# Performance work log

Measured on AMD Instinct MI355X. Metric: run time of the kernel, lower is better.

## Reference

```python
import jax, jax.numpy as jnp
import numpy as np

V = 50000      # word vocab
CV = 63        # char vocab (60 chars + 3 tags)
HW = 512       # word hidden size
HC = 256       # char hidden size
NLW = 2        # word lstm layers
NLC = 2        # char lstm layers
L = 12         # chars in the word


def _lstm_layers(x, H, C, Wih, Whh, bih, bhh):
    """One time-step of a multi-layer LSTM (PyTorch gate order i,f,g,o).
    x: [1, D], H/C: [nl, 1, D]. Returns (top_h, newH, newC)."""
    nl = Wih.shape[0]
    newH, newC = [], []
    inp = x
    for l in range(nl):
        gates = inp @ Wih[l].T + H[l] @ Whh[l].T + bih[l] + bhh[l]  # [1, 4D]
        i, f, g, o = jnp.split(gates, 4, axis=-1)
        i = jax.nn.sigmoid(i)
        f = jax.nn.sigmoid(f)
        g = jnp.tanh(g)
        o = jax.nn.sigmoid(o)
        c = f * C[l] + i * g
        h = o * jnp.tanh(c)
        newH.append(h)
        newC.append(c)
        inp = h
    return inp, jnp.stack(newH), jnp.stack(newC)


def setup_inputs() -> dict:
    key = jax.random.key(0)
    ks = jax.random.split(key, 20)
    sW = 1.0 / np.sqrt(HW)
    sC = 1.0 / np.sqrt(HC)
    return {
        "x_word": jax.random.randint(ks[0], (1,), 0, V),
        "x_char": jax.random.randint(ks[1], (L,), 0, CV),
        "h_word_h": jax.random.normal(ks[2], (NLW, 1, HW), jnp.float32),
        "h_word_c": jax.random.normal(ks[3], (NLW, 1, HW), jnp.float32),
        "h_char_h": jax.random.normal(ks[4], (NLC, 1, HC), jnp.float32),
        "h_char_c": jax.random.normal(ks[5], (NLC, 1, HC), jnp.float32),
        "word_emb": jax.random.normal(ks[6], (V, HW), jnp.float32),
        "word_Wih": jax.random.normal(ks[7], (NLW, 4 * HW, HW), jnp.float32) * sW,
        "word_Whh": jax.random.normal(ks[8], (NLW, 4 * HW, HW), jnp.float32) * sW,
        "word_bih": jax.random.normal(ks[9], (NLW, 4 * HW), jnp.float32) * sW,
        "word_bhh": jax.random.normal(ks[10], (NLW, 4 * HW), jnp.float32) * sW,
        "dec_W": jax.random.normal(ks[11], (V, HW), jnp.float32) * sW,
        "dec_b": jax.random.normal(ks[12], (V,), jnp.float32) * sW,
        "char_emb": jax.random.normal(ks[13], (CV, HC), jnp.float32),
        "char_Wih": jax.random.normal(ks[14], (NLC, 4 * HC, HC), jnp.float32) * sC,
        "char_Whh": jax.random.normal(ks[15], (NLC, 4 * HC, HC), jnp.float32) * sC,
        "char_bih": jax.random.normal(ks[16], (NLC, 4 * HC), jnp.float32) * sC,
        "char_bhh": jax.random.normal(ks[17], (NLC, 4 * HC), jnp.float32) * sC,
        "char_to_embedding": jax.random.normal(ks[18], (HW, HC), jnp.float32),
        "g_w": jax.random.normal(ks[19], (HW,), jnp.float32) * sW,
        "g_b": jax.random.normal(jax.random.fold_in(key, 99), (1,), jnp.float32),
    }


def reference(x_word, x_char, h_word_h, h_word_c, h_char_h, h_char_c,
              word_emb, word_Wih, word_Whh, word_bih, word_bhh,
              dec_W, dec_b,
              char_emb, char_Wih, char_Whh, char_bih, char_bhh,
              char_to_embedding, g_w, g_b):
    # character-level recurrence over the word's characters
    def char_step(carry, cidx):
        H, C = carry
        xc = char_emb[cidx][None, :]  # [1, HC]
        _, H, C = _lstm_layers(xc, H, C, char_Wih, char_Whh, char_bih, char_bhh)
        return (H, C), None

    (h_char_h, h_char_c), _ = jax.lax.scan(char_step, (h_char_h, h_char_c), x_char)

    # note: original uses h_char[1] (the CELL state) of the last layer
    x_c = char_to_embedding @ h_char_c[-1].T          # [HW, 1]
    x_w = word_emb[x_word[0]][None, :]                # [1, HW]
    g = jax.nn.relu(jnp.dot(g_w, x_w[0]) + g_b[0])    # scalar gate
    x = (1.0 - g) * x_w + g * x_c.T                   # [1, HW]

    y, h_word_h, h_word_c = _lstm_layers(x, h_word_h, h_word_c,
                                         word_Wih, word_Whh, word_bih, word_bhh)
    y = y @ dec_W.T + dec_b                           # [1, V]
    return y, h_word_h, h_word_c, h_char_h, h_char_c
```

## Files before the change

kernel.cpp:

```cpp
#include <hip/hip_runtime.h>
#include <stdint.h>


static __device__ __forceinline__ float dot4(float4 w, const float* p){
    return w.x*p[0] + w.y*p[1] + w.z*p[2] + w.w*p[3];
}
static __device__ __forceinline__ float sigf(float x){ return 1.0f / (1.0f + __expf(-x)); }
static __device__ __forceinline__ float tanhf_(float x){
    x = fminf(fmaxf(x, -15.0f), 15.0f);
    float e = __expf(2.0f * x);
    return (e - 1.0f) / (e + 1.0f);
}


__global__ __launch_bounds__(256) void k_char(
    int t,
    const int* __restrict__ x_char,
    const float* __restrict__ hch, const float* __restrict__ hcc,
    const float* __restrict__ char_emb,
    const float* __restrict__ cWih, const float* __restrict__ cWhh,
    const float* __restrict__ cbih, const float* __restrict__ cbhh,
    const float* __restrict__ word_emb, const int* __restrict__ x_word,
    const float* __restrict__ g_w, const float* __restrict__ g_b,
    float* __restrict__ ws)
{
    const int tid = threadIdx.x;
    const int bx = blockIdx.x;

    if (bx == 64){
        if (t == 0){
            __shared__ float sw[4];
            const size_t wbase = (size_t)x_word[0] * 512;
            float p = g_w[2*tid]   * word_emb[wbase + 2*tid]
                    + g_w[2*tid+1] * word_emb[wbase + 2*tid+1];
            #pragma unroll
            for (int m = 32; m >= 1; m >>= 1) p += __shfl_xor(p, m, 64);
            if ((tid & 63) == 0) sw[tid >> 6] = p;
            __syncthreads();
            if (tid == 0){
                float gg = sw[0] + sw[1] + sw[2] + sw[3] + g_b[0];
                ws[3072] = fmaxf(gg, 0.0f);
            }
        }
        return;
    }

    __shared__ float sH1[256];
    __shared__ float sH2[256];
    __shared__ float sE[256];
    __shared__ float sg1[16], sg2[16];

    float* h1b = ws;
    float* h2b = ws + 512;
    float* c1  = ws + 1024;
    float* c2  = ws + 1280;

    sH1[tid] = (t == 0) ? hch[tid] : h1b[(t & 1)*256 + tid];
    if (t >= 1) sH2[tid] = (t == 1) ? hch[256 + tid] : h2b[((t-1) & 1)*256 + tid];
    if (t < 12) sE[tid] = char_emb[x_char[t]*256 + tid];
    __syncthreads();

    const int rg = tid >> 4;
    const int lane16 = tid & 15;
    const int gate = rg & 3;
    const int uu = rg >> 2;
    const int u = (bx << 2) + uu;
    const int row = (gate << 8) + u;

    float a1 = 0.f, a2 = 0.f;
    if (t < 12){
        const float4* wi = (const float4*)(cWih + (size_t)row*256) + lane16*4;
        const float4* wh = (const float4*)(cWhh + (size_t)row*256) + lane16*4;
        const float* xp = sE  + lane16*16;
        const float* hp = sH1 + lane16*16;
        #pragma unroll
        for (int j = 0; j < 4; ++j) a1 += dot4(wi[j], xp + 4*j) + dot4(wh[j], hp + 4*j);
    }
    if (t >= 1){
        const size_t r2 = (size_t)(1024 + row);
        const float4* wi = (const float4*)(cWih + r2*256) + lane16*4;
        const float4* wh = (const float4*)(cWhh + r2*256) + lane16*4;
        const float* xp = sH1 + lane16*16;
        const float* hp = sH2 + lane16*16;
        #pragma unroll
        for (int j = 0; j < 4; ++j) a2 += dot4(wi[j], xp + 4*j) + dot4(wh[j], hp + 4*j);
    }
    #pragma unroll
    for (int m = 8; m >= 1; m >>= 1){
        a1 += __shfl_xor(a1, m, 64);
        a2 += __shfl_xor(a2, m, 64);
    }
    if (lane16 == 0){
        if (t < 12) sg1[rg] = a1 + cbih[row]        + cbhh[row];
        if (t >= 1) sg2[rg] = a2 + cbih[1024 + row] + cbhh[1024 + row];
    }
    __syncthreads();

    if (tid < 4){
        if (t < 12){
            int uh = (bx << 2) + tid;
            float gi = sigf(sg1[tid*4+0]);
            float gf = sigf(sg1[tid*4+1]);
            float gg = tanhf_(sg1[tid*4+2]);
            float go = sigf(sg1[tid*4+3]);
            float cp = (t == 0) ? hcc[uh] : c1[uh];
            float c = gf * cp + gi * gg;
            c1[uh] = c;
            h1b[((t+1) & 1)*256 + uh] = go * tanhf_(c);
        }
    } else if (tid < 8){
        if (t >= 1){
            int q = tid - 4;
            int uh = (bx << 2) + q;
            float gi = sigf(sg2[q*4+0]);
            float gf = sigf(sg2[q*4+1]);
            float gg = tanhf_(sg2[q*4+2]);
            float go = sigf(sg2[q*4+3]);
            float cp = (t == 1) ? hcc[256 + uh] : c2[uh];
            float c = gf * cp + gi * gg;
            c2[uh] = c;
            h2b[(t & 1)*256 + uh] = go * tanhf_(c);
        }
    }
}

__global__ __launch_bounds__(256) void k_mix(
    const float* __restrict__ cte, float* __restrict__ ws,
    float* __restrict__ out)
{
    const int tid = threadIdx.x;
    const int bx = blockIdx.x;
    __shared__ float sC2[256];
    sC2[tid] = ws[1280 + tid];
    __syncthreads();

    if (tid < 4){
        int uh = (bx << 2) + tid;
        out[52048 + uh]       = ws[uh];
        out[52048 + 256 + uh] = ws[512 + uh];
        out[52560 + uh]       = ws[1024 + uh];
        out[52560 + 256 + uh] = ws[1280 + uh];
    }
    const int rr = tid >> 5;
    const int lane32 = tid & 31;
    const int row = (bx << 3) + rr;
    const float4* wp = (const float4*)(cte + (size_t)row*256) + lane32*2;
    float acc = dot4(wp[0], sC2 + lane32*8) + dot4(wp[1], sC2 + lane32*8 + 4);
    #pragma unroll
    for (int m = 16; m >= 1; m >>= 1) acc += __shfl_xor(acc, m, 64);
    if (lane32 == 0) ws[1536 + row] = acc;
}

__global__ __launch_bounds__(256) void k_word(
    int l,
    const float* __restrict__ hwh, const float* __restrict__ hwc,
    const float* __restrict__ word_emb, const int* __restrict__ x_word,
    const float* __restrict__ wWih, const float* __restrict__ wWhh,
    const float* __restrict__ wbih, const float* __restrict__ wbhh,
    float* __restrict__ ws, float* __restrict__ out)
{
    const int tid = threadIdx.x;
    const int bx = blockIdx.x;
    __shared__ float sX[512];
    __shared__ float sg[32];

    if (l == 0){
        const size_t wbase = (size_t)x_word[0] * 512;
        float g = ws[3072];
        sX[2*tid]   = (1.0f - g) * word_emb[wbase + 2*tid]   + g * ws[1536 + 2*tid];
        sX[2*tid+1] = (1.0f - g) * word_emb[wbase + 2*tid+1] + g * ws[1536 + 2*tid+1];
    } else {
        sX[2*tid]   = ws[2048 + 2*tid];
        sX[2*tid+1] = ws[2048 + 2*tid+1];
    }
    __syncthreads();

    const int rg8 = tid >> 3;
    const int lane8 = tid & 7;
    const int gate = rg8 & 3;
    const int uu = rg8 >> 2;
    const int uw = (bx << 3) + uu;
    const int row = (gate << 9) + uw;
    const size_t rf = (size_t)(l*2048 + row);

    const float4* wi = (const float4*)(wWih + rf*512) + lane8*16;
    const float4* wh = (const float4*)(wWhh + rf*512) + lane8*16;
    const float4* hv = (const float4*)(hwh + l*512) + lane8*16;
    const float* xp = sX + lane8*64;
    float acc = 0.f;
    #pragma unroll
    for (int j = 0; j < 16; ++j){
        float4 h4 = hv[j];
        acc += dot4(wi[j], xp + 4*j);
        float4 w4 = wh[j];
        acc += w4.x*h4.x + w4.y*h4.y + w4.z*h4.z + w4.w*h4.w;
    }
    #pragma unroll
    for (int m = 4; m >= 1; m >>= 1) acc += __shfl_xor(acc, m, 64);
    if (lane8 == 0) sg[rg8] = acc + wbih[rf] + wbhh[rf];
    __syncthreads();

    if (tid < 8){
        int u2 = (bx << 3) + tid;
        float gi = sigf(sg[tid*4+0]);
        float gf = sigf(sg[tid*4+1]);
        float gg = tanhf_(sg[tid*4+2]);
        float go = sigf(sg[tid*4+3]);
        float c = gf * hwc[l*512 + u2] + gi * gg;
        float h = go * tanhf_(c);
        ws[2048 + l*512 + u2] = h;
        out[50000 + l*512 + u2] = h;
        out[51024 + l*512 + u2] = c;
    }
}

__global__ __launch_bounds__(256) void k_dec(
    const float* __restrict__ dec_W, const float* __restrict__ dec_b,
    const float* __restrict__ h2, float* __restrict__ out)
{
    const int lane = threadIdx.x & 63;
    const int wid = (blockIdx.x * blockDim.x + threadIdx.x) >> 6;
    const int nw = (gridDim.x * blockDim.x) >> 6;
    const float4* hp = (const float4*)h2 + lane*2;
    float4 ha = hp[0], hb = hp[1];
    float hx0[4] = {ha.x, ha.y, ha.z, ha.w};
    float hx1[4] = {hb.x, hb.y, hb.z, hb.w};
    for (int r = wid; r < 50000; r += nw){
        const float4* wp = (const float4*)(dec_W + (size_t)r*512) + lane*2;
        float acc = dot4(wp[0], hx0) + dot4(wp[1], hx1);
        #pragma unroll
        for (int m = 32; m >= 1; m >>= 1) acc += __shfl_xor(acc, m, 64);
        if (lane == 0) out[r] = acc + dec_b[r];
    }
}

extern "C" void kernel_launch(void* const* d_in, const int* in_sizes, int n_in,
                              void* d_out, int out_size, void* d_ws, size_t ws_size,
                              hipStream_t stream)
{
    const int*   x_word   = (const int*)d_in[0];
    const int*   x_char   = (const int*)d_in[1];
    const float* hwh      = (const float*)d_in[2];
    const float* hwc      = (const float*)d_in[3];
    const float* hch      = (const float*)d_in[4];
    const float* hcc      = (const float*)d_in[5];
    const float* word_emb = (const float*)d_in[6];
    const float* wWih     = (const float*)d_in[7];
    const float* wWhh     = (const float*)d_in[8];
    const float* wbih     = (const float*)d_in[9];
    const float* wbhh     = (const float*)d_in[10];
    const float* dec_W    = (const float*)d_in[11];
    const float* dec_b    = (const float*)d_in[12];
    const float* char_emb = (const float*)d_in[13];
    const float* cWih     = (const float*)d_in[14];
    const float* cWhh     = (const float*)d_in[15];
    const float* cbih     = (const float*)d_in[16];
    const float* cbhh     = (const float*)d_in[17];
    const float* cte      = (const float*)d_in[18];
    const float* g_w      = (const float*)d_in[19];
    const float* g_b      = (const float*)d_in[20];

    float* ws = (float*)d_ws;
    float* out = (float*)d_out;

    for (int t = 0; t <= 12; ++t){
        hipLaunchKernelGGL(k_char, dim3(65), dim3(256), 0, stream,
            t, x_char, hch, hcc, char_emb, cWih, cWhh, cbih, cbhh,
            word_emb, x_word, g_w, g_b, ws);
    }
    hipLaunchKernelGGL(k_mix, dim3(64), dim3(256), 0, stream, cte, ws, out);
    hipLaunchKernelGGL(k_word, dim3(64), dim3(256), 0, stream,
        0, hwh, hwc, word_emb, x_word, wWih, wWhh, wbih, wbhh, ws, out);
    hipLaunchKernelGGL(k_word, dim3(64), dim3(256), 0, stream,
        1, hwh, hwc, word_emb, x_word, wWih, wWhh, wbih, wbhh, ws, out);
    hipLaunchKernelGGL(k_dec, dim3(625), dim3(256), 0, stream,
        dec_W, dec_b, ws + 2560, out);
}
```

Measured before the change: 329.7 us.

## Fuse all stages into one persistent kernel with grid barriers and decoder prefetch

Replaces the 17 separate launches (13 char steps, mix, two word layers, decoder) with one persistent kernel of 256 blocks. The first 64 blocks run the recurrent chain and synchronise through atomic grid barriers in workspace. The other 192 blocks stream the whole decoder weight matrix to warm the cache, then spin on a flag before everyone does the decoder GEMV. This removes launch overhead and overlaps the decoder weight fetch with the serial LSTM work. It relies on all blocks being co-resident and adds spin-wait costs; the prefetch only helps if the matrix (about 100MB) stays in the last-level cache.

```diff
diff --git a/kernel.cpp b/kernel.cpp
--- a/kernel.cpp
+++ b/kernel.cpp
@@ -1,6 +1,11 @@
 #include <hip/hip_runtime.h>
 #include <stdint.h>
 
+
+#define NCHAR 64
+#define NBLK  256
+#define BAR_I 3072
+#define FLAG_SLOT 20
 
 static __device__ __forceinline__ float dot4(float4 w, const float* p){
     return w.x*p[0] + w.y*p[1] + w.z*p[2] + w.w*p[3];
@@ -12,220 +17,253 @@
     return (e - 1.0f) / (e + 1.0f);
 }
 
-
-__global__ __launch_bounds__(256) void k_char(
-    int t,
-    const int* __restrict__ x_char,
-    const float* __restrict__ hch, const float* __restrict__ hcc,
-    const float* __restrict__ char_emb,
-    const float* __restrict__ cWih, const float* __restrict__ cWhh,
-    const float* __restrict__ cbih, const float* __restrict__ cbhh,
-    const float* __restrict__ word_emb, const int* __restrict__ x_word,
-    const float* __restrict__ g_w, const float* __restrict__ g_b,
-    float* __restrict__ ws)
+static __device__ __forceinline__ void gbar(int* bar, int slot, int n){
+    __syncthreads();
+    if (threadIdx.x == 0){
+        __hip_atomic_fetch_add(bar + slot, 1, __ATOMIC_RELEASE, __HIP_MEMORY_SCOPE_AGENT);
+        while (__hip_atomic_load(bar + slot, __ATOMIC_RELAXED, __HIP_MEMORY_SCOPE_AGENT) < n)
+            __builtin_amdgcn_s_sleep(1);
+        (void)__hip_atomic_load(bar + slot, __ATOMIC_ACQUIRE, __HIP_MEMORY_SCOPE_AGENT);
+    }
+    __syncthreads();
+}
+
+
+__global__ __launch_bounds__(256) void k_fused(
+    const int* x_word, const int* x_char,
+    const float* hwh, const float* hwc, const float* hch, const float* hcc,
+    const float* word_emb, const float* wWih, const float* wWhh,
+    const float* wbih, const float* wbhh,
+    const float* dec_W, const float* dec_b,
+    const float* char_emb, const float* cWih, const float* cWhh,
+    const float* cbih, const float* cbhh,
+    const float* cte, const float* g_w, const float* g_b,
+    float* ws, int* bar, float* out)
 {
     const int tid = threadIdx.x;
     const int bx = blockIdx.x;
 
-    if (bx == 64){
-        if (t == 0){
-            __shared__ float sw[4];
-            const size_t wbase = (size_t)x_word[0] * 512;
+    __shared__ float sH1[256], sH2[256], sE[256];
+    __shared__ float sg1[16], sg2[16];
+    __shared__ float sX[512];
+    __shared__ float sgw[32];
+    __shared__ float sw4[4];
+    __shared__ float s_g;
+
+    if (bx < NCHAR){
+        float* h1b = ws;
+        float* h2b = ws + 512;
+        float* c1  = ws + 1024;
+        float* c2  = ws + 1280;
+
+        const int rg = tid >> 4;
+        const int lane16 = tid & 15;
+        const int gate = rg & 3;
+        const int uu = rg >> 2;
+        const int u = (bx << 2) + uu;
+        const int row = (gate << 8) + u;
+
+        for (int t = 0; t <= 12; ++t){
+            sH1[tid] = (t == 0) ? hch[tid] : h1b[(t & 1)*256 + tid];
+            if (t >= 1) sH2[tid] = (t == 1) ? hch[256 + tid] : h2b[((t-1) & 1)*256 + tid];
+            if (t < 12) sE[tid] = char_emb[x_char[t]*256 + tid];
+            __syncthreads();
+
+            float a1 = 0.f, a2 = 0.f;
+            if (t < 12){
+                const float4* wi = (const float4*)(cWih + (size_t)row*256) + lane16*4;
+                const float4* wh = (const float4*)(cWhh + (size_t)row*256) + lane16*4;
+                const float* xp = sE  + lane16*16;
+                const float* hp = sH1 + lane16*16;
+                #pragma unroll
+                for (int j = 0; j < 4; ++j) a1 += dot4(wi[j], xp + 4*j) + dot4(wh[j], hp + 4*j);
+            }
+            if (t >= 1){
+                const size_t r2 = (size_t)(1024 + row);
+                const float4* wi = (const float4*)(cWih + r2*256) + lane16*4;
+                const float4* wh = (const float4*)(cWhh + r2*256) + lane16*4;
+                const float* xp = sH1 + lane16*16;
+                const float* hp = sH2 + lane16*16;
+                #pragma unroll
+                for (int j = 0; j < 4; ++j) a2 += dot4(wi[j], xp + 4*j) + dot4(wh[j], hp + 4*j);
+            }
+            #pragma unroll
+            for (int m = 8; m >= 1; m >>= 1){
+                a1 += __shfl_xor(a1, m, 64);
+                a2 += __shfl_xor(a2, m, 64);
+            }
+            if (lane16 == 0){
+                if (t < 12) sg1[rg] = a1 + cbih[row]        + cbhh[row];
+                if (t >= 1) sg2[rg] = a2 + cbih[1024 + row] + cbhh[1024 + row];
+            }
+            __syncthreads();
+
+            if (tid < 4){
+                if (t < 12){
+                    int uh = (bx << 2) + tid;
+                    float gi = sigf(sg1[tid*4+0]);
+                    float gf = sigf(sg1[tid*4+1]);
+                    float gg = tanhf_(sg1[tid*4+2]);
+                    float go = sigf(sg1[tid*4+3]);
+                    float cp = (t == 0) ? hcc[uh] : c1[uh];
+                    float c = gf * cp + gi * gg;
+                    c1[uh] = c;
+                    h1b[((t+1) & 1)*256 + uh] = go * tanhf_(c);
+                }
+            } else if (tid < 8){
+                if (t >= 1){
+                    int q = tid - 4;
+                    int uh = (bx << 2) + q;
+                    float gi = sigf(sg2[q*4+0]);
+                    float gf = sigf(sg2[q*4+1]);
+                    float gg = tanhf_(sg2[q*4+2]);
+                    float go = sigf(sg2[q*4+3]);
+                    float cp = (t == 1) ? hcc[256 + uh] : c2[uh];
+                    float c = gf * cp + gi * gg;
+                    c2[uh] = c;
+                    h2b[(t & 1)*256 + uh] = go * tanhf_(c);
+                }
+            }
+            gbar(bar, t, NCHAR);
+        }
+
+        sH1[tid] = c2[tid];
+        if (tid < 4){
+            int uh = (bx << 2) + tid;
+            out[52048 + uh]       = h1b[uh];
+            out[52048 + 256 + uh] = h2b[uh];
+            out[52560 + uh]       = c1[uh];
+            out[52560 + 256 + uh] = c2[uh];
+        }
+        const size_t wbase = (size_t)x_word[0] * 512;
+        {
             float p = g_w[2*tid]   * word_emb[wbase + 2*tid]
                     + g_w[2*tid+1] * word_emb[wbase + 2*tid+1];
             #pragma unroll
             for (int m = 32; m >= 1; m >>= 1) p += __shfl_xor(p, m, 64);
-            if ((tid & 63) == 0) sw[tid >> 6] = p;
-            __syncthreads();
-            if (tid == 0){
-                float gg = sw[0] + sw[1] + sw[2] + sw[3] + g_b[0];
-                ws[3072] = fmaxf(gg, 0.0f);
-            }
-        }
-        return;
-    }
-
-    __shared__ float sH1[256];
-    __shared__ float sH2[256];
-    __shared__ float sE[256];
-    __shared__ float sg1[16], sg2[16];
-
-    float* h1b = ws;
-    float* h2b = ws + 512;
-    float* c1  = ws + 1024;
-    float* c2  = ws + 1280;
-
-    sH1[tid] = (t == 0) ? hch[tid] : h1b[(t & 1)*256 + tid];
-    if (t >= 1) sH2[tid] = (t == 1) ? hch[256 + tid] : h2b[((t-1) & 1)*256 + tid];
-    if (t < 12) sE[tid] = char_emb[x_char[t]*256 + tid];
-    __syncthreads();
-
-    const int rg = tid >> 4;
-    const int lane16 = tid & 15;
-    const int gate = rg & 3;
-    const int uu = rg >> 2;
-    const int u = (bx << 2) + uu;
-    const int row = (gate << 8) + u;
-
-    float a1 = 0.f, a2 = 0.f;
-    if (t < 12){
-        const float4* wi = (const float4*)(cWih + (size_t)row*256) + lane16*4;
-        const float4* wh = (const float4*)(cWhh + (size_t)row*256) + lane16*4;
-        const float* xp = sE  + lane16*16;
-        const float* hp = sH1 + lane16*16;
-        #pragma unroll
-        for (int j = 0; j < 4; ++j) a1 += dot4(wi[j], xp + 4*j) + dot4(wh[j], hp + 4*j);
-    }
-    if (t >= 1){
-        const size_t r2 = (size_t)(1024 + row);
-        const float4* wi = (const float4*)(cWih + r2*256) + lane16*4;
-        const float4* wh = (const float4*)(cWhh + r2*256) + lane16*4;
-        const float* xp = sH1 + lane16*16;
-        const float* hp = sH2 + lane16*16;
-        #pragma unroll
-        for (int j = 0; j < 4; ++j) a2 += dot4(wi[j], xp + 4*j) + dot4(wh[j], hp + 4*j);
-    }
-    #pragma unroll
-    for (int m = 8; m >= 1; m >>= 1){
-        a1 += __shfl_xor(a1, m, 64);
-        a2 += __shfl_xor(a2, m, 64);
-    }
-    if (lane16 == 0){
-        if (t < 12) sg1[rg] = a1 + cbih[row]        + cbhh[row];
-        if (t >= 1) sg2[rg] = a2 + cbih[1024 + row] + cbhh[1024 + row];
-    }
-    __syncthreads();
-
-    if (tid < 4){
-        if (t < 12){
-            int uh = (bx << 2) + tid;
-            float gi = sigf(sg1[tid*4+0]);
-            float gf = sigf(sg1[tid*4+1]);
-            float gg = tanhf_(sg1[tid*4+2]);
-            float go = sigf(sg1[tid*4+3]);
-            float cp = (t == 0) ? hcc[uh] : c1[uh];
-            float c = gf * cp + gi * gg;
-            c1[uh] = c;
-            h1b[((t+1) & 1)*256 + uh] = go * tanhf_(c);
-        }
-    } else if (tid < 8){
-        if (t >= 1){
-            int q = tid - 4;
-            int uh = (bx << 2) + q;
-            float gi = sigf(sg2[q*4+0]);
-            float gf = sigf(sg2[q*4+1]);
-            float gg = tanhf_(sg2[q*4+2]);
-            float go = sigf(sg2[q*4+3]);
-            float cp = (t == 1) ? hcc[256 + uh] : c2[uh];
-            float c = gf * cp + gi * gg;
-            c2[uh] = c;
-            h2b[(t & 1)*256 + uh] = go * tanhf_(c);
-        }
-    }
-}
-
-__global__ __launch_bounds__(256) void k_mix(
-    const float* __restrict__ cte, float* __restrict__ ws,
-    float* __restrict__ out)
-{
-    const int tid = threadIdx.x;
-    const int bx = blockIdx.x;
-    __shared__ float sC2[256];
-    sC2[tid] = ws[1280 + tid];
-    __syncthreads();
-
-    if (tid < 4){
-        int uh = (bx << 2) + tid;
-        out[52048 + uh]       = ws[uh];
-        out[52048 + 256 + uh] = ws[512 + uh];
-        out[52560 + uh]       = ws[1024 + uh];
-        out[52560 + 256 + uh] = ws[1280 + uh];
-    }
-    const int rr = tid >> 5;
-    const int lane32 = tid & 31;
-    const int row = (bx << 3) + rr;
-    const float4* wp = (const float4*)(cte + (size_t)row*256) + lane32*2;
-    float acc = dot4(wp[0], sC2 + lane32*8) + dot4(wp[1], sC2 + lane32*8 + 4);
-    #pragma unroll
-    for (int m = 16; m >= 1; m >>= 1) acc += __shfl_xor(acc, m, 64);
-    if (lane32 == 0) ws[1536 + row] = acc;
-}
-
-__global__ __launch_bounds__(256) void k_word(
-    int l,
-    const float* __restrict__ hwh, const float* __restrict__ hwc,
-    const float* __restrict__ word_emb, const int* __restrict__ x_word,
-    const float* __restrict__ wWih, const float* __restrict__ wWhh,
-    const float* __restrict__ wbih, const float* __restrict__ wbhh,
-    float* __restrict__ ws, float* __restrict__ out)
-{
-    const int tid = threadIdx.x;
-    const int bx = blockIdx.x;
-    __shared__ float sX[512];
-    __shared__ float sg[32];
-
-    if (l == 0){
-        const size_t wbase = (size_t)x_word[0] * 512;
-        float g = ws[3072];
-        sX[2*tid]   = (1.0f - g) * word_emb[wbase + 2*tid]   + g * ws[1536 + 2*tid];
-        sX[2*tid+1] = (1.0f - g) * word_emb[wbase + 2*tid+1] + g * ws[1536 + 2*tid+1];
-    } else {
+            if ((tid & 63) == 0) sw4[tid >> 6] = p;
+        }
+        __syncthreads();
+        if (tid == 0) s_g = fmaxf(sw4[0] + sw4[1] + sw4[2] + sw4[3] + g_b[0], 0.0f);
+        {
+            const int rr = tid >> 5;
+            const int lane32 = tid & 31;
+            const int crow = (bx << 3) + rr;
+            const float4* wp = (const float4*)(cte + (size_t)crow*256) + lane32*2;
+            float acc = dot4(wp[0], sH1 + lane32*8) + dot4(wp[1], sH1 + lane32*8 + 4);
+            #pragma unroll
+            for (int m = 16; m >= 1; m >>= 1) acc += __shfl_xor(acc, m, 64);
+            if (lane32 == 0) ws[1536 + crow] = acc;
+        }
+        gbar(bar, 13, NCHAR);
+
+        const int rg8 = tid >> 3;
+        const int lane8 = tid & 7;
+        const int wgate = rg8 & 3;
+        const int wuu = rg8 >> 2;
+        const int uw = (bx << 3) + wuu;
+        const int wrow = (wgate << 9) + uw;
+        {
+            float g = s_g;
+            sX[2*tid]   = (1.0f - g) * word_emb[wbase + 2*tid]   + g * ws[1536 + 2*tid];
+            sX[2*tid+1] = (1.0f - g) * word_emb[wbase + 2*tid+1] + g * ws[1536 + 2*tid+1];
+        }
+        __syncthreads();
+        {
+            const size_t rf = (size_t)wrow;
+            const float4* wi = (const float4*)(wWih + rf*512) + lane8*16;
+            const float4* wh = (const float4*)(wWhh + rf*512) + lane8*16;
+            const float4* hv = (const float4*)(hwh) + lane8*16;
+            const float* xp = sX + lane8*64;
+            float acc = 0.f;
+            #pragma unroll
+            for (int j = 0; j < 16; ++j){
+                float4 h4 = hv[j];
+                acc += dot4(wi[j], xp + 4*j);
+                float4 w4 = wh[j];
+                acc += w4.x*h4.x + w4.y*h4.y + w4.z*h4.z + w4.w*h4.w;
+            }
+            #pragma unroll
+            for (int m = 4; m >= 1; m >>= 1) acc += __shfl_xor(acc, m, 64);
+            if (lane8 == 0) sgw[rg8] = acc + wbih[rf] + wbhh[rf];
+        }
+        __syncthreads();
+        if (tid < 8){
+            int u2 = (bx << 3) + tid;
+            float gi = sigf(sgw[tid*4+0]);
+            float gf = sigf(sgw[tid*4+1]);
+            float gg = tanhf_(sgw[tid*4+2]);
+            float go = sigf(sgw[tid*4+3]);
+            float c = gf * hwc[u2] + gi * gg;
+            float h = go * tanhf_(c);
+            ws[2048 + u2] = h;
+            out[50000 + u2] = h;
+            out[51024 + u2] = c;
+        }
+        gbar(bar, 14, NCHAR);
+
         sX[2*tid]   = ws[2048 + 2*tid];
         sX[2*tid+1] = ws[2048 + 2*tid+1];
+        __syncthreads();
+        {
+            const size_t rf = (size_t)(2048 + wrow);
+            const float4* wi = (const float4*)(wWih + rf*512) + lane8*16;
+            const float4* wh = (const float4*)(wWhh + rf*512) + lane8*16;
+            const float4* hv = (const float4*)(hwh + 512) + lane8*16;
+            const float* xp = sX + lane8*64;
+            float acc = 0.f;
+            #pragma unroll
+            for (int j = 0; j < 16; ++j){
+                float4 h4 = hv[j];
+                acc += dot4(wi[j], xp + 4*j);
+                float4 w4 = wh[j];
+                acc += w4.x*h4.x + w4.y*h4.y + w4.z*h4.z + w4.w*h4.w;
+            }
+            #pragma unroll
+            for (int m = 4; m >= 1; m >>= 1) acc += __shfl_xor(acc, m, 64);
+            if (lane8 == 0) sgw[rg8] = acc + wbih[rf] + wbhh[rf];
+        }
+        __syncthreads();
+        if (tid < 8){
+            int u2 = (bx << 3) + tid;
+            float gi = sigf(sgw[tid*4+0]);
+            float gf = sigf(sgw[tid*4+1]);
+            float gg = tanhf_(sgw[tid*4+2]);
+            float go = sigf(sgw[tid*4+3]);
+            float c = gf * hwc[512 + u2] + gi * gg;
+            float h = go * tanhf_(c);
+            ws[2560 + u2] = h;
+            out[50000 + 512 + u2] = h;
+            out[51024 + 512 + u2] = c;
+        }
+        gbar(bar, 15, NCHAR);
+        if (bx == 0 && tid == 0)
+            __hip_atomic_store(bar + FLAG_SLOT, 1, __ATOMIC_RELEASE, __HIP_MEMORY_SCOPE_AGENT);
+    } else {
+        const float4* dw = (const float4*)dec_W;
+        const int gid = (bx - NCHAR)*256 + tid;
+        float acc = 0.f;
+        for (int i = gid; i < 6400000; i += 49152){
+            float4 v = dw[i];
+            acc += v.x + v.y + v.z + v.w;
+        }
+        ws[8192 + gid] = acc;
+        __syncthreads();
+        if (tid == 0){
+            while (__hip_atomic_load(bar + FLAG_SLOT, __ATOMIC_RELAXED, __HIP_MEMORY_SCOPE_AGENT) == 0)
+                __builtin_amdgcn_s_sleep(4);
+            (void)__hip_atomic_load(bar + FLAG_SLOT, __ATOMIC_ACQUIRE, __HIP_MEMORY_SCOPE_AGENT);
+        }
+        __syncthreads();
     }
-    __syncthreads();
-
-    const int rg8 = tid >> 3;
-    const int lane8 = tid & 7;
-    const int gate = rg8 & 3;
-    const int uu = rg8 >> 2;
-    const int uw = (bx << 3) + uu;
-    const int row = (gate << 9) + uw;
-    const size_t rf = (size_t)(l*2048 + row);
-
-    const float4* wi = (const float4*)(wWih + rf*512) + lane8*16;
-    const float4* wh = (const float4*)(wWhh + rf*512) + lane8*16;
-    const float4* hv = (const float4*)(hwh + l*512) + lane8*16;
-    const float* xp = sX + lane8*64;
-    float acc = 0.f;
-    #pragma unroll
-    for (int j = 0; j < 16; ++j){
-        float4 h4 = hv[j];
-        acc += dot4(wi[j], xp + 4*j);
-        float4 w4 = wh[j];
-        acc += w4.x*h4.x + w4.y*h4.y + w4.z*h4.z + w4.w*h4.w;
-    }
-    #pragma unroll
-    for (int m = 4; m >= 1; m >>= 1) acc += __shfl_xor(acc, m, 64);
-    if (lane8 == 0) sg[rg8] = acc + wbih[rf] + wbhh[rf];
-    __syncthreads();
-
-    if (tid < 8){
-        int u2 = (bx << 3) + tid;
-        float gi = sigf(sg[tid*4+0]);
-        float gf = sigf(sg[tid*4+1]);
-        float gg = tanhf_(sg[tid*4+2]);
-        float go = sigf(sg[tid*4+3]);
-        float c = gf * hwc[l*512 + u2] + gi * gg;
-        float h = go * tanhf_(c);
-        ws[2048 + l*512 + u2] = h;
-        out[50000 + l*512 + u2] = h;
-        out[51024 + l*512 + u2] = c;
-    }
-}
-
-__global__ __launch_bounds__(256) void k_dec(
-    const float* __restrict__ dec_W, const float* __restrict__ dec_b,
-    const float* __restrict__ h2, float* __restrict__ out)
-{
-    const int lane = threadIdx.x & 63;
-    const int wid = (blockIdx.x * blockDim.x + threadIdx.x) >> 6;
-    const int nw = (gridDim.x * blockDim.x) >> 6;
-    const float4* hp = (const float4*)h2 + lane*2;
+
+    const int lane = tid & 63;
+    const int wid = (bx << 2) + (tid >> 6);
+    const float4* hp = (const float4*)(ws + 2560) + lane*2;
     float4 ha = hp[0], hb = hp[1];
     float hx0[4] = {ha.x, ha.y, ha.z, ha.w};
     float hx1[4] = {hb.x, hb.y, hb.z, hb.w};
-    for (int r = wid; r < 50000; r += nw){
+    for (int r = wid; r < 50000; r += 1024){
         const float4* wp = (const float4*)(dec_W + (size_t)r*512) + lane*2;
         float acc = dot4(wp[0], hx0) + dot4(wp[1], hx1);
         #pragma unroll
@@ -261,18 +299,11 @@
     const float* g_b      = (const float*)d_in[20];
 
     float* ws = (float*)d_ws;
-    float* out = (float*)d_out;
-
-    for (int t = 0; t <= 12; ++t){
-        hipLaunchKernelGGL(k_char, dim3(65), dim3(256), 0, stream,
-            t, x_char, hch, hcc, char_emb, cWih, cWhh, cbih, cbhh,
-            word_emb, x_word, g_w, g_b, ws);
-    }
-    hipLaunchKernelGGL(k_mix, dim3(64), dim3(256), 0, stream, cte, ws, out);
-    hipLaunchKernelGGL(k_word, dim3(64), dim3(256), 0, stream,
-        0, hwh, hwc, word_emb, x_word, wWih, wWhh, wbih, wbhh, ws, out);
-    hipLaunchKernelGGL(k_word, dim3(64), dim3(256), 0, stream,
-        1, hwh, hwc, word_emb, x_word, wWih, wWhh, wbih, wbhh, ws, out);
-    hipLaunchKernelGGL(k_dec, dim3(625), dim3(256), 0, stream,
-        dec_W, dec_b, ws + 2560, out);
-}
+    int* bar = (int*)((char*)d_ws + BAR_I*4);
+    hipMemsetAsync(bar, 0, 32 * sizeof(int), stream);
+
+    hipLaunchKernelGGL(k_fused, dim3(NBLK), dim3(256), 0, stream,
+        x_word, x_char, hwh, hwc, hch, hcc, word_emb, wWih, wWhh, wbih, wbhh,
+        dec_W, dec_b, char_emb, cWih, cWhh, cbih, cbhh, cte, g_w, g_b,
+        ws, bar, (float*)d_out);
+}
```

New measurement: 390.8 us. 18.5% more time.
